# Performance work log

Hardware: AMD Instinct MI355X
Metric: run time of the kernel (lower is better)

## Reference

```python
import jax, jax.numpy as jnp
import numpy as np

B, IN, H, O, L, G = 4096, 512, 1024, 256, 2, 3


def _lin_init(key, out_dim, in_dim):
    k1, k2 = jax.random.split(key)
    bound = 1.0 / np.sqrt(in_dim)
    w = jax.random.uniform(k1, (out_dim, in_dim), jnp.float32, -bound, bound)
    b = jax.random.uniform(k2, (out_dim,), jnp.float32, -bound, bound)
    return w, b


def setup_inputs() -> dict:
    key = jax.random.key(0)
    ks = jax.random.split(key, 10)
    x = jax.random.normal(ks[0], (B, IN), jnp.float32)
    hidden = jax.random.normal(ks[1], (L, B, H), jnp.float32)
    i2d_w, i2d_b = _lin_init(ks[2], H, IN)
    # stacked GRU params, PyTorch gate order (r, z, n); layer0 input dim == H (after i2d)
    kih = jax.random.split(ks[3], L)
    khh = jax.random.split(ks[4], L)
    gru_w_ih = jnp.stack([_lin_init(kih[l], 3 * H, H)[0] for l in range(L)])
    gru_b_ih = jnp.stack([_lin_init(kih[l], 3 * H, H)[1] for l in range(L)])
    gru_w_hh = jnp.stack([_lin_init(khh[l], 3 * H, H)[0] for l in range(L)])
    gru_b_hh = jnp.stack([_lin_init(khh[l], 3 * H, H)[1] for l in range(L)])
    mu_w, mu_b = _lin_init(ks[5], O * G, H)
    sigma_w, sigma_b = _lin_init(ks[6], O * G, H)
    pi_w, pi_b = _lin_init(ks[7], O * G, H)
    return {"x": x, "hidden": hidden, "i2d_w": i2d_w, "i2d_b": i2d_b,
            "gru_w_ih": gru_w_ih, "gru_w_hh": gru_w_hh,
            "gru_b_ih": gru_b_ih, "gru_b_hh": gru_b_hh,
            "mu_w": mu_w, "mu_b": mu_b, "sigma_w": sigma_w, "sigma_b": sigma_b,
            "pi_w": pi_w, "pi_b": pi_b, "batch_size": B}


def reference(x, hidden, i2d_w, i2d_b, gru_w_ih, gru_w_hh, gru_b_ih, gru_b_hh,
              mu_w, mu_b, sigma_w, sigma_b, pi_w, pi_b, batch_size):
    # input projection + relu
    h1 = jax.nn.relu(x @ i2d_w.T + i2d_b)  # [B, H]
    # single-timestep stacked GRU (PyTorch cell math, gate order r,z,n)
    inp = h1
    new_h = []
    for l in range(hidden.shape[0]):
        h_prev = hidden[l]
        gi = inp @ gru_w_ih[l].T + gru_b_ih[l]   # [B, 3H]
        gh = h_prev @ gru_w_hh[l].T + gru_b_hh[l]
        i_r, i_z, i_n = jnp.split(gi, 3, axis=-1)
        h_r, h_z, h_n = jnp.split(gh, 3, axis=-1)
        r = jax.nn.sigmoid(i_r + h_r)
        z = jax.nn.sigmoid(i_z + h_z)
        n = jnp.tanh(i_n + r * h_n)
        h_new = (1.0 - z) * n + z * h_prev
        new_h.append(h_new)
        inp = h_new
    hidden_out = jnp.stack(new_h)            # [L, B, H]
    h_out = jnp.tanh(inp)                    # [B, H]
    n_g = 3
    o = mu_w.shape[0] // n_g
    pi = jax.nn.softmax((h_out @ pi_w.T + pi_b).reshape(-1, n_g, o), axis=1)
    mu = (h_out @ mu_w.T + mu_b).reshape(-1, n_g, o)
    sig = jax.nn.softplus(h_out @ sigma_w.T + sigma_b).reshape(-1, n_g, o)
    return (mu, sig, pi, hidden_out)
```

## Files before the change

kernel.cpp:

```cpp
#include <hip/hip_runtime.h>
#include <stdint.h>

typedef unsigned short bf16u;
typedef float f32x4 __attribute__((ext_vector_type(4)));
typedef short bf16x8 __attribute__((ext_vector_type(8)));
typedef float f4 __attribute__((ext_vector_type(4)));

#define AS1 __attribute__((address_space(1)))
#define AS3 __attribute__((address_space(3)))

__device__ __forceinline__ float b2f(bf16u u) {
  union { uint32_t i; float f; } v; v.i = ((uint32_t)u) << 16; return v.f;
}
__device__ __forceinline__ uint32_t f2b(float f) {
  union { float f; uint32_t i; } v; v.f = f;
  uint32_t i = v.i;
  return (i + 0x7FFFu + ((i >> 16) & 1u)) >> 16;
}
__device__ __forceinline__ float sigm(float x) { return 1.f / (1.f + __expf(-x)); }
__device__ __forceinline__ float ftanh(float x) {
  float e = __expf(2.f * x);
  return 1.f - 2.f / (e + 1.f);
}
__device__ __forceinline__ uint4 pack8(f4 a, f4 b) {
  uint4 o;
  o.x = (f2b(a[0]) & 0xffffu) | (f2b(a[1]) << 16);
  o.y = (f2b(a[2]) & 0xffffu) | (f2b(a[3]) << 16);
  o.z = (f2b(b[0]) & 0xffffu) | (f2b(b[1]) << 16);
  o.w = (f2b(b[2]) & 0xffffu) | (f2b(b[3]) << 16);
  return o;
}

struct CvtSeg { const float* src; char* dst; int blk0; int count; int tobf16; };
struct CvtArgs { CvtSeg s[12]; int nseg; };

__global__ __launch_bounds__(256)
void cvt_multi(CvtArgs a) {
  int b = blockIdx.x, seg = 0;
  while (seg + 1 < a.nseg && b >= a.s[seg + 1].blk0) ++seg;
  const CvtSeg& S = a.s[seg];
  size_t idx = ((size_t)(b - S.blk0) * 2048) + (size_t)threadIdx.x * 8;
  if ((long long)idx >= S.count) return;
  f4 x = *(const f4*)&S.src[idx];
  f4 y = *(const f4*)&S.src[idx + 4];
  if (S.tobf16) {
    *(uint4*)((bf16u*)S.dst + idx) = pack8(x, y);
  } else {
    *(f4*)((float*)S.dst + idx) = x;
    *(f4*)((float*)S.dst + idx + 4) = y;
  }
}

__global__ __launch_bounds__(256)
void gemm_i2d(const float* __restrict__ xf, const bf16u* __restrict__ W,
              const float* __restrict__ bias, bf16u* __restrict__ Cout) {
  constexpr int K = 512, N = 1024;
  __shared__ bf16u sA[64 * 64];
  __shared__ bf16u sB[128 * 64];
  const int tid = threadIdx.x, wave = tid >> 6, lane = tid & 63;
  const int bn = blockIdx.x, bm = blockIdx.y;

  const int srA = wave * 16 + (lane >> 3);
  const int srB = wave * 32 + (lane >> 3);
  const int kc  = (lane & 7) ^ ((lane >> 3) & 7);
  const float* gx = xf + (size_t)(bm * 64 + srA) * K + kc * 8;
  const bf16u* wg = W + (size_t)(bn * 128 + srB) * K + kc * 8;
  const int adst = srA * 64 + (lane & 7) * 8;

  const int wm = wave >> 1, wn = wave & 1;
  const int q = lane >> 4, cl = lane & 15;

  int aoff[2][2], boff[4][2];
#pragma unroll
  for (int i = 0; i < 2; ++i) {
    int m = wm * 32 + i * 16 + cl;
#pragma unroll
    for (int kk = 0; kk < 2; ++kk)
      aoff[i][kk] = m * 64 + (((q + kk * 4) ^ (m & 7)) * 8);
  }
#pragma unroll
  for (int j = 0; j < 4; ++j) {
    int n = wn * 64 + j * 16 + cl;
#pragma unroll
    for (int kk = 0; kk < 2; ++kk)
      boff[j][kk] = n * 64 + (((q + kk * 4) ^ (n & 7)) * 8);
  }

  f32x4 acc[2][4] = {};
  for (int k0 = 0; k0 < K; k0 += 64) {
    f4 a0 = *(const f4*)(gx + k0);
    f4 a1 = *(const f4*)(gx + k0 + 4);
    f4 a2 = *(const f4*)(gx + (size_t)8 * K + k0);
    f4 a3 = *(const f4*)(gx + (size_t)8 * K + k0 + 4);
#pragma unroll
    for (int t = 0; t < 4; ++t)
      __builtin_amdgcn_global_load_lds(
          (const AS1 void*)(wg + k0 + (size_t)t * 8 * K),
          (AS3 void*)&sB[wave * 2048 + t * 512], 16, 0, 0);
    *(uint4*)&sA[adst]       = pack8(a0, a1);
    *(uint4*)&sA[adst + 512] = pack8(a2, a3);
    __syncthreads();
#pragma unroll
    for (int kk = 0; kk < 2; ++kk) {
      bf16x8 af[2], bfr[4];
#pragma unroll
      for (int i = 0; i < 2; ++i) af[i] = *(const bf16x8*)&sA[aoff[i][kk]];
#pragma unroll
      for (int j = 0; j < 4; ++j) bfr[j] = *(const bf16x8*)&sB[boff[j][kk]];
#pragma unroll
      for (int i = 0; i < 2; ++i)
#pragma unroll
        for (int j = 0; j < 4; ++j)
          acc[i][j] = __builtin_amdgcn_mfma_f32_16x16x32_bf16(af[i], bfr[j], acc[i][j], 0, 0, 0);
    }
    __syncthreads();
  }

  float bv[4];
#pragma unroll
  for (int j = 0; j < 4; ++j)
    bv[j] = bias[bn * 128 + wn * 64 + j * 16 + cl];

  const int row0 = bm * 64 + wm * 32 + q * 4;
  const int col0 = bn * 128 + wn * 64 + cl;
#pragma unroll
  for (int i = 0; i < 2; ++i)
#pragma unroll
    for (int j = 0; j < 4; ++j)
#pragma unroll
      for (int r = 0; r < 4; ++r) {
        float v = fmaxf(acc[i][j][r] + bv[j], 0.f);
        Cout[(size_t)(row0 + i * 16 + r) * N + (col0 + j * 16)] = (bf16u)f2b(v);
      }
}

template <int LAST>
__global__ __launch_bounds__(512)
void gru_fused(const bf16u* __restrict__ inp, const bf16u* __restrict__ hpb,
               const bf16u* __restrict__ wih, const bf16u* __restrict__ whh,
               const float* __restrict__ bih, const float* __restrict__ bhh,
               const float* __restrict__ hpf, float* __restrict__ hid_out,
               bf16u* __restrict__ nxt) {
  constexpr int K = 1024;
  __shared__ bf16u s[640 * 64];
  const int tid  = threadIdx.x;
  const int wave = tid >> 6;
  const int lane = tid & 63;
  const int bn = blockIdx.x, bm = blockIdx.y;
  const int c0 = bn * 64;

  const int rr  = tid >> 3;
  const int kc  = (tid & 7) ^ (rr & 7);
  const int dst0 = rr * 64 + (tid & 7) * 8;
  const bf16u* gI = inp + (size_t)(bm * 128 + rr) * K + kc * 8;
  const bf16u* gH = hpb + (size_t)(bm * 128 + rr) * K + kc * 8;
  const bf16u* gW[6];
#pragma unroll
  for (int p = 0; p < 6; ++p) {
    const bf16u* base = (p < 3) ? wih : whh;
    gW[p] = base + (size_t)((p % 3) * 1024 + c0 + rr) * K + kc * 8;
  }

  const int wm = wave >> 1, wn = wave & 1;
  const int q = lane >> 4, cl = lane & 15;

  int aoff[2][2], boff[2][2];
#pragma unroll
  for (int i = 0; i < 2; ++i) {
    int ai = wm * 32 + i * 16 + cl;
#pragma unroll
    for (int kk = 0; kk < 2; ++kk)
      aoff[i][kk] = ai * 64 + (((q + kk * 4) ^ (ai & 7)) * 8);
  }
#pragma unroll
  for (int j = 0; j < 2; ++j) {
    int br = wn * 32 + j * 16 + cl;
#pragma unroll
    for (int kk = 0; kk < 2; ++kk)
      boff[j][kk] = (256 + br) * 64 + (((q + kk * 4) ^ (br & 7)) * 8);
  }

  f32x4 acc[6][2][2] = {};

  for (int k0 = 0; k0 < K; k0 += 64) {
    __builtin_amdgcn_global_load_lds((const AS1 void*)(gI + k0),
        (AS3 void*)&s[dst0], 16, 0, 0);
    __builtin_amdgcn_global_load_lds((const AS1 void*)(gI + k0 + (size_t)64 * K),
        (AS3 void*)&s[dst0 + 4096], 16, 0, 0);
    __builtin_amdgcn_global_load_lds((const AS1 void*)(gH + k0),
        (AS3 void*)&s[dst0 + 8192], 16, 0, 0);
    __builtin_amdgcn_global_load_lds((const AS1 void*)(gH + k0 + (size_t)64 * K),
        (AS3 void*)&s[dst0 + 12288], 16, 0, 0);
#pragma unroll
    for (int p = 0; p < 6; ++p)
      __builtin_amdgcn_global_load_lds((const AS1 void*)(gW[p] + k0),
          (AS3 void*)&s[dst0 + (4 + p) * 4096], 16, 0, 0);
    __syncthreads();
#pragma unroll
    for (int kk = 0; kk < 2; ++kk) {
      bf16x8 aI[2], aH[2];
#pragma unroll
      for (int i = 0; i < 2; ++i) {
        aI[i] = *(const bf16x8*)&s[aoff[i][kk]];
        aH[i] = *(const bf16x8*)&s[aoff[i][kk] + 8192];
      }
#pragma unroll
      for (int p = 0; p < 6; ++p) {
        bf16x8 b0 = *(const bf16x8*)&s[boff[0][kk] + p * 4096];
        bf16x8 b1 = *(const bf16x8*)&s[boff[1][kk] + p * 4096];
        if (p < 3) {
          acc[p][0][0] = __builtin_amdgcn_mfma_f32_16x16x32_bf16(aI[0], b0, acc[p][0][0], 0, 0, 0);
          acc[p][0][1] = __builtin_amdgcn_mfma_f32_16x16x32_bf16(aI[0], b1, acc[p][0][1], 0, 0, 0);
          acc[p][1][0] = __builtin_amdgcn_mfma_f32_16x16x32_bf16(aI[1], b0, acc[p][1][0], 0, 0, 0);
          acc[p][1][1] = __builtin_amdgcn_mfma_f32_16x16x32_bf16(aI[1], b1, acc[p][1][1], 0, 0, 0);
        } else {
          acc[p][0][0] = __builtin_amdgcn_mfma_f32_16x16x32_bf16(aH[0], b0, acc[p][0][0], 0, 0, 0);
          acc[p][0][1] = __builtin_amdgcn_mfma_f32_16x16x32_bf16(aH[0], b1, acc[p][0][1], 0, 0, 0);
          acc[p][1][0] = __builtin_amdgcn_mfma_f32_16x16x32_bf16(aH[1], b0, acc[p][1][0], 0, 0, 0);
          acc[p][1][1] = __builtin_amdgcn_mfma_f32_16x16x32_bf16(aH[1], b1, acc[p][1][1], 0, 0, 0);
        }
      }
    }
    __syncthreads();
  }

  float bI[3][2], bH[3][2];
#pragma unroll
  for (int g = 0; g < 3; ++g)
#pragma unroll
    for (int j = 0; j < 2; ++j) {
      int col = c0 + wn * 32 + j * 16 + cl;
      bI[g][j] = bih[g * 1024 + col];
      bH[g][j] = bhh[g * 1024 + col];
    }

#pragma unroll
  for (int i = 0; i < 2; ++i)
#pragma unroll
    for (int j = 0; j < 2; ++j)
#pragma unroll
      for (int r_ = 0; r_ < 4; ++r_) {
        int row = bm * 128 + wm * 32 + i * 16 + q * 4 + r_;
        int col = c0 + wn * 32 + j * 16 + cl;
        size_t o = (size_t)row * 1024 + col;
        float vir = acc[0][i][j][r_] + bI[0][j];
        float viz = acc[1][i][j][r_] + bI[1][j];
        float vin = acc[2][i][j][r_] + bI[2][j];
        float vhr = acc[3][i][j][r_] + bH[0][j];
        float vhz = acc[4][i][j][r_] + bH[1][j];
        float vhn = acc[5][i][j][r_] + bH[2][j];
        float rg = sigm(vir + vhr);
        float zg = sigm(viz + vhz);
        float ng = ftanh(vin + rg * vhn);
        float hnew = (1.f - zg) * ng + zg * hpf[o];
        hid_out[o] = hnew;
        nxt[o] = (bf16u)f2b(LAST ? ftanh(hnew) : hnew);
      }
}

__global__ __launch_bounds__(512)
void gemm_heads3(const bf16u* __restrict__ A, const bf16u* __restrict__ Wp,
                 const float* __restrict__ biasp, float* __restrict__ out_mu,
                 float* __restrict__ out_sg, float* __restrict__ out_pi) {
  constexpr int K = 1024;
  __shared__ bf16u s[320 * 64];
  const int tid = threadIdx.x, wave = tid >> 6, lane = tid & 63;
  const int bn = blockIdx.x, bm = blockIdx.y;
  const bool ispi = (bn >= 12);
  const int o0 = (bn - 12) * 64;
  const int nbt = ispi ? 3 : 2;
  const int nj  = ispi ? 6 : 4;

  const int rr  = tid >> 3;
  const int kc  = (tid & 7) ^ (rr & 7);
  const int dst0 = rr * 64 + (tid & 7) * 8;
  const bf16u* gA = A + (size_t)(bm * 128 + rr) * K + kc * 8;
  const bf16u* gB[3];
#pragma unroll
  for (int t = 0; t < 3; ++t) {
    int wrow = ispi ? (1536 + t * 256 + o0 + rr) : (bn * 128 + t * 64 + rr);
    gB[t] = Wp + (size_t)wrow * K + kc * 8;
  }

  const int wm = wave >> 1, wn = wave & 1;
  const int q = lane >> 4, cl = lane & 15;

  int aoff[2][2], boff[6][2];
#pragma unroll
  for (int i = 0; i < 2; ++i) {
    int m = wm * 32 + i * 16 + cl;
#pragma unroll
    for (int kk = 0; kk < 2; ++kk)
      aoff[i][kk] = m * 64 + (((q + kk * 4) ^ (m & 7)) * 8);
  }
#pragma unroll
  for (int j = 0; j < 6; ++j) {
    int l = ispi ? ((j >> 1) * 64 + wn * 32 + (j & 1) * 16 + cl)
                 : (wn * 64 + (j & 3) * 16 + cl);
#pragma unroll
    for (int kk = 0; kk < 2; ++kk)
      boff[j][kk] = 8192 + l * 64 + (((q + kk * 4) ^ (l & 7)) * 8);
  }

  f32x4 acc[2][6] = {};
  for (int k0 = 0; k0 < K; k0 += 64) {
    __builtin_amdgcn_global_load_lds((const AS1 void*)(gA + k0),
        (AS3 void*)&s[dst0], 16, 0, 0);
    __builtin_amdgcn_global_load_lds((const AS1 void*)(gA + k0 + (size_t)64 * K),
        (AS3 void*)&s[dst0 + 4096], 16, 0, 0);
#pragma unroll
    for (int t = 0; t < 3; ++t)
      if (t < nbt)
        __builtin_amdgcn_global_load_lds((const AS1 void*)(gB[t] + k0),
            (AS3 void*)&s[8192 + dst0 + t * 4096], 16, 0, 0);
    __syncthreads();
#pragma unroll
    for (int kk = 0; kk < 2; ++kk) {
      bf16x8 af[2];
#pragma unroll
      for (int i = 0; i < 2; ++i) af[i] = *(const bf16x8*)&s[aoff[i][kk]];
#pragma unroll
      for (int j = 0; j < 6; ++j) {
        if (j >= nj) continue;
        bf16x8 bf_ = *(const bf16x8*)&s[boff[j][kk]];
#pragma unroll
        for (int i = 0; i < 2; ++i)
          acc[i][j] = __builtin_amdgcn_mfma_f32_16x16x32_bf16(af[i], bf_, acc[i][j], 0, 0, 0);
      }
    }
    __syncthreads();
  }

  const int row0 = bm * 128 + wm * 32 + q * 4;
  if (!ispi) {
    float bv[4];
#pragma unroll
    for (int j = 0; j < 4; ++j)
      bv[j] = biasp[bn * 128 + wn * 64 + j * 16 + cl];
    const int head = bn / 6;
    const int ch0 = (bn % 6) * 128 + wn * 64 + cl;
#pragma unroll
    for (int i = 0; i < 2; ++i)
#pragma unroll
      for (int j = 0; j < 4; ++j)
#pragma unroll
        for (int r = 0; r < 4; ++r) {
          float v = acc[i][j][r] + bv[j];
          size_t off = (size_t)(row0 + i * 16 + r) * 768 + (ch0 + j * 16);
          if (head == 0) out_mu[off] = v;
          else out_sg[off] = fmaxf(v, 0.f) + __logf(1.f + __expf(-fabsf(v)));
        }
  } else {
    float bv[6];
#pragma unroll
    for (int j = 0; j < 6; ++j)
      bv[j] = biasp[1536 + (j >> 1) * 256 + o0 + wn * 32 + (j & 1) * 16 + cl];
#pragma unroll
    for (int i = 0; i < 2; ++i)
#pragma unroll
      for (int jo = 0; jo < 2; ++jo)
#pragma unroll
        for (int r = 0; r < 4; ++r) {
          float v0 = acc[i][jo][r]     + bv[jo];
          float v1 = acc[i][2 + jo][r] + bv[2 + jo];
          float v2 = acc[i][4 + jo][r] + bv[4 + jo];
          float m = fmaxf(fmaxf(v0, v1), v2);
          float e0 = __expf(v0 - m), e1 = __expf(v1 - m), e2 = __expf(v2 - m);
          float sc = 1.f / (e0 + e1 + e2);
          size_t base = (size_t)(row0 + i * 16 + r) * 768
                        + (o0 + wn * 32 + jo * 16 + cl);
          out_pi[base]       = e0 * sc;
          out_pi[base + 256] = e1 * sc;
          out_pi[base + 512] = e2 * sc;
        }
  }
}

extern "C" void kernel_launch(void* const* d_in, const int* in_sizes, int n_in,
                              void* d_out, int out_size, void* d_ws, size_t ws_size,
                              hipStream_t stream) {
  const float* x      = (const float*)d_in[0];
  const float* hidden = (const float*)d_in[1];
  const float* i2d_w  = (const float*)d_in[2];
  const float* i2d_b  = (const float*)d_in[3];
  const float* w_ih   = (const float*)d_in[4];
  const float* w_hh   = (const float*)d_in[5];
  const float* b_ih   = (const float*)d_in[6];
  const float* b_hh   = (const float*)d_in[7];
  const float* mu_w   = (const float*)d_in[8];
  const float* mu_b   = (const float*)d_in[9];
  const float* sg_w   = (const float*)d_in[10];
  const float* sg_b   = (const float*)d_in[11];
  const float* pi_w   = (const float*)d_in[12];
  const float* pi_b   = (const float*)d_in[13];
  float* out = (float*)d_out;

  const size_t BH = 4194304;
  const int HS = 3145728;
  float* hid_base = out + (size_t)3 * HS;

  dim3 blk(256, 1, 1);

  bf16u* wb_i2d = (bf16u*)d_ws;
  bf16u* wb_ih  = wb_i2d + 524288;
  bf16u* wb_hh  = wb_ih + 6291456;
  bf16u* wb_hd  = wb_hh + 6291456;
  float* biasp  = (float*)((char*)d_ws + 30932992);
  const size_t wbytes = 30942208;

  bf16u* hb0 = (bf16u*)((char*)d_ws + wbytes);
  bf16u* hb1 = hb0 + BH;
  const size_t hbbytes = (size_t)2 * BH * 2;

  {
    CvtArgs a{};
    int nb = 0;
    auto seg = [&](const float* s, void* d, int count, int tobf) {
      a.s[a.nseg++] = {s, (char*)d, nb, count, tobf};
      nb += (count + 2047) / 2048;
    };
    seg(i2d_w, wb_i2d, 524288, 1);
    seg(w_ih,  wb_ih, 6291456, 1);
    seg(w_hh,  wb_hh, 6291456, 1);
    seg(mu_w,  wb_hd, 786432, 1);
    seg(sg_w,  wb_hd + 786432, 786432, 1);
    seg(pi_w,  wb_hd + 1572864, 786432, 1);
    seg(mu_b,  biasp, 768, 0);
    seg(sg_b,  biasp + 768, 768, 0);
    seg(pi_b,  biasp + 1536, 768, 0);
    seg(hidden, hb0, 8388608, 1);
    cvt_multi<<<dim3(nb), blk, 0, stream>>>(a);
  }

  int Bc = 4096;
  while (wbytes + hbbytes + (size_t)Bc * 4096 > ws_size && Bc > 256) Bc >>= 1;
  const int nchunk = 4096 / Bc;

  char* cbase = (char*)d_ws + wbytes + hbbytes;
  bf16u* ws0  = (bf16u*)cbase;
  bf16u* nxt0 = (bf16u*)(cbase + (size_t)Bc * 2048);

  for (int c = 0; c < nchunk; ++c) {
    const size_t off = (size_t)c * Bc;
    const float* h0_c = hidden + off * 1024;
    const float* h1_c = hidden + BH + off * 1024;

    gemm_i2d<<<dim3(8, Bc / 64), blk, 0, stream>>>(
        x + off * 512, wb_i2d, i2d_b, ws0);
    gru_fused<0><<<dim3(16, Bc / 128), dim3(512, 1, 1), 0, stream>>>(
        ws0, hb0 + off * 1024, wb_ih, wb_hh, b_ih, b_hh, h0_c,
        hid_base + off * 1024, nxt0);
    gru_fused<1><<<dim3(16, Bc / 128), dim3(512, 1, 1), 0, stream>>>(
        nxt0, hb1 + off * 1024, wb_ih + 3145728, wb_hh + 3145728,
        b_ih + 3072, b_hh + 3072, h1_c, hid_base + BH + off * 1024, ws0);
    gemm_heads3<<<dim3(16, Bc / 128), dim3(512, 1, 1), 0, stream>>>(
        ws0, wb_hd, biasp, out + off * 768, out + HS + off * 768,
        out + 2 * (size_t)HS + off * 768);
  }
}
```

Baseline: 360.7 us.

## Double-buffer GRU fused kernel LDS staging with K-tile 32 and async prefetch

```diff
diff --git a/kernel.cpp b/kernel.cpp
--- a/kernel.cpp
+++ b/kernel.cpp
@@ -142,87 +142,101 @@
                const float* __restrict__ hpf, float* __restrict__ hid_out,
                bf16u* __restrict__ nxt) {
   constexpr int K = 1024;
-  __shared__ bf16u s[640 * 64];
+  constexpr int NT = K / 32;
+  __shared__ bf16u s[2][640 * 32];
   const int tid  = threadIdx.x;
   const int wave = tid >> 6;
   const int lane = tid & 63;
   const int bn = blockIdx.x, bm = blockIdx.y;
   const int c0 = bn * 64;
 
-  const int rr  = tid >> 3;
-  const int kc  = (tid & 7) ^ (rr & 7);
-  const int dst0 = rr * 64 + (tid & 7) * 8;
-  const bf16u* gI = inp + (size_t)(bm * 128 + rr) * K + kc * 8;
-  const bf16u* gH = hpb + (size_t)(bm * 128 + rr) * K + kc * 8;
-  const bf16u* gW[6];
-#pragma unroll
-  for (int p = 0; p < 6; ++p) {
-    const bf16u* base = (p < 3) ? wih : whh;
-    gW[p] = base + (size_t)((p % 3) * 1024 + c0 + rr) * K + kc * 8;
+  const int rr2  = tid >> 2;
+  const int slot = tid & 3;
+  const int kc   = slot ^ (rr2 & 3);
+  const int dst0 = rr2 * 32 + slot * 8;
+  const bf16u* gI = inp + (size_t)(bm * 128 + rr2) * K + kc * 8;
+  const bf16u* gH = hpb + (size_t)(bm * 128 + rr2) * K + kc * 8;
+  const bf16u* gWl[3];
+  {
+    const int pr = rr2 & 63, hi = rr2 >> 6;
+#pragma unroll
+    for (int L = 0; L < 3; ++L) {
+      const int pidx = L * 2 + hi;
+      const bf16u* base = (pidx < 3) ? wih : whh;
+      gWl[L] = base + (size_t)((pidx % 3) * 1024 + c0 + pr) * K + kc * 8;
+    }
   }
 
   const int wm = wave >> 1, wn = wave & 1;
   const int q = lane >> 4, cl = lane & 15;
 
-  int aoff[2][2], boff[2][2];
+  int aoff[2], boff[6][2];
 #pragma unroll
   for (int i = 0; i < 2; ++i) {
-    int ai = wm * 32 + i * 16 + cl;
-#pragma unroll
-    for (int kk = 0; kk < 2; ++kk)
-      aoff[i][kk] = ai * 64 + (((q + kk * 4) ^ (ai & 7)) * 8);
-  }
-#pragma unroll
-  for (int j = 0; j < 2; ++j) {
-    int br = wn * 32 + j * 16 + cl;
-#pragma unroll
-    for (int kk = 0; kk < 2; ++kk)
-      boff[j][kk] = (256 + br) * 64 + (((q + kk * 4) ^ (br & 7)) * 8);
-  }
+    const int ai = wm * 32 + i * 16 + cl;
+    aoff[i] = ai * 32 + ((q ^ (ai & 3)) * 8);
+  }
+#pragma unroll
+  for (int p = 0; p < 6; ++p)
+#pragma unroll
+    for (int j = 0; j < 2; ++j) {
+      const int br = wn * 32 + j * 16 + cl;
+      boff[p][j] = 8192 + (p * 64 + br) * 32 + ((q ^ (br & 3)) * 8);
+    }
 
   f32x4 acc[6][2][2] = {};
 
-  for (int k0 = 0; k0 < K; k0 += 64) {
-    __builtin_amdgcn_global_load_lds((const AS1 void*)(gI + k0),
-        (AS3 void*)&s[dst0], 16, 0, 0);
-    __builtin_amdgcn_global_load_lds((const AS1 void*)(gI + k0 + (size_t)64 * K),
-        (AS3 void*)&s[dst0 + 4096], 16, 0, 0);
-    __builtin_amdgcn_global_load_lds((const AS1 void*)(gH + k0),
-        (AS3 void*)&s[dst0 + 8192], 16, 0, 0);
-    __builtin_amdgcn_global_load_lds((const AS1 void*)(gH + k0 + (size_t)64 * K),
-        (AS3 void*)&s[dst0 + 12288], 16, 0, 0);
-#pragma unroll
-    for (int p = 0; p < 6; ++p)
-      __builtin_amdgcn_global_load_lds((const AS1 void*)(gW[p] + k0),
-          (AS3 void*)&s[dst0 + (4 + p) * 4096], 16, 0, 0);
-    __syncthreads();
-#pragma unroll
-    for (int kk = 0; kk < 2; ++kk) {
-      bf16x8 aI[2], aH[2];
-#pragma unroll
-      for (int i = 0; i < 2; ++i) {
-        aI[i] = *(const bf16x8*)&s[aoff[i][kk]];
-        aH[i] = *(const bf16x8*)&s[aoff[i][kk] + 8192];
+#define STG(buf, t)                                                           \
+  do {                                                                        \
+    __builtin_amdgcn_global_load_lds((const AS1 void*)(gI + (t) * 32),        \
+        (AS3 void*)&s[buf][dst0], 16, 0, 0);                                  \
+    __builtin_amdgcn_global_load_lds((const AS1 void*)(gH + (t) * 32),        \
+        (AS3 void*)&s[buf][4096 + dst0], 16, 0, 0);                           \
+    _Pragma("unroll")                                                         \
+    for (int L = 0; L < 3; ++L)                                               \
+      __builtin_amdgcn_global_load_lds((const AS1 void*)(gWl[L] + (t) * 32),  \
+          (AS3 void*)&s[buf][8192 + L * 4096 + dst0], 16, 0, 0);              \
+  } while (0)
+
+  STG(0, 0);
+  for (int t = 0; t < NT; ++t) {
+    const int cb = t & 1;
+    if (t + 1 < NT) {
+      STG(cb ^ 1, t + 1);
+      asm volatile("s_waitcnt vmcnt(5)" ::: "memory");
+    } else {
+      asm volatile("s_waitcnt vmcnt(0)" ::: "memory");
+    }
+    __builtin_amdgcn_s_barrier();
+    asm volatile("" ::: "memory");
+    bf16x8 aI[2], aH[2];
+#pragma unroll
+    for (int i = 0; i < 2; ++i) {
+      aI[i] = *(const bf16x8*)&s[cb][aoff[i]];
+      aH[i] = *(const bf16x8*)&s[cb][aoff[i] + 4096];
+    }
+    __builtin_amdgcn_s_setprio(1);
+#pragma unroll
+    for (int p = 0; p < 6; ++p) {
+      bf16x8 b0 = *(const bf16x8*)&s[cb][boff[p][0]];
+      bf16x8 b1 = *(const bf16x8*)&s[cb][boff[p][1]];
+      if (p < 3) {
+        acc[p][0][0] = __builtin_amdgcn_mfma_f32_16x16x32_bf16(aI[0], b0, acc[p][0][0], 0, 0, 0);
+        acc[p][0][1] = __builtin_amdgcn_mfma_f32_16x16x32_bf16(aI[0], b1, acc[p][0][1], 0, 0, 0);
+        acc[p][1][0] = __builtin_amdgcn_mfma_f32_16x16x32_bf16(aI[1], b0, acc[p][1][0], 0, 0, 0);
+        acc[p][1][1] = __builtin_amdgcn_mfma_f32_16x16x32_bf16(aI[1], b1, acc[p][1][1], 0, 0, 0);
+      } else {
+        acc[p][0][0] = __builtin_amdgcn_mfma_f32_16x16x32_bf16(aH[0], b0, acc[p][0][0], 0, 0, 0);
+        acc[p][0][1] = __builtin_amdgcn_mfma_f32_16x16x32_bf16(aH[0], b1, acc[p][0][1], 0, 0, 0);
+        acc[p][1][0] = __builtin_amdgcn_mfma_f32_16x16x32_bf16(aH[1], b0, acc[p][1][0], 0, 0, 0);
+        acc[p][1][1] = __builtin_amdgcn_mfma_f32_16x16x32_bf16(aH[1], b1, acc[p][1][1], 0, 0, 0);
       }
-#pragma unroll
-      for (int p = 0; p < 6; ++p) {
-        bf16x8 b0 = *(const bf16x8*)&s[boff[0][kk] + p * 4096];
-        bf16x8 b1 = *(const bf16x8*)&s[boff[1][kk] + p * 4096];
-        if (p < 3) {
-          acc[p][0][0] = __builtin_amdgcn_mfma_f32_16x16x32_bf16(aI[0], b0, acc[p][0][0], 0, 0, 0);
-          acc[p][0][1] = __builtin_amdgcn_mfma_f32_16x16x32_bf16(aI[0], b1, acc[p][0][1], 0, 0, 0);
-          acc[p][1][0] = __builtin_amdgcn_mfma_f32_16x16x32_bf16(aI[1], b0, acc[p][1][0], 0, 0, 0);
-          acc[p][1][1] = __builtin_amdgcn_mfma_f32_16x16x32_bf16(aI[1], b1, acc[p][1][1], 0, 0, 0);
-        } else {
-          acc[p][0][0] = __builtin_amdgcn_mfma_f32_16x16x32_bf16(aH[0], b0, acc[p][0][0], 0, 0, 0);
-          acc[p][0][1] = __builtin_amdgcn_mfma_f32_16x16x32_bf16(aH[0], b1, acc[p][0][1], 0, 0, 0);
-          acc[p][1][0] = __builtin_amdgcn_mfma_f32_16x16x32_bf16(aH[1], b0, acc[p][1][0], 0, 0, 0);
-          acc[p][1][1] = __builtin_amdgcn_mfma_f32_16x16x32_bf16(aH[1], b1, acc[p][1][1], 0, 0, 0);
-        }
-      }
-    }
-    __syncthreads();
-  }
+    }
+    __builtin_amdgcn_s_setprio(0);
+    __builtin_amdgcn_s_barrier();
+    asm volatile("" ::: "memory");
+  }
+#undef STG
 
   float bI[3][2], bH[3][2];
 #pragma unroll
```

Measured after the change: 362.9 us. Within noise of the previous version (+0.6%).
